# Kernel tuning notes

Hardware: AMD Instinct MI355X
Metric: run time of the kernel (lower is better)

The kernel has to match this reference:

```python
import jax, jax.numpy as jnp
import numpy as np

N_NODES = 100000
NFEAT = 256
NHID = 8
HEADS = 8
NCLASS = 32
N_EDGES = 1600000
NEG_SLOPE = 0.2


def setup_inputs() -> dict:
    key = jax.random.key(0)
    ks = jax.random.split(key, 10)
    glorot = lambda k, shape: jax.random.uniform(
        k, shape, jnp.float32, -1.0, 1.0) * np.sqrt(6.0 / (shape[0] + shape[-1]))
    x = jax.random.normal(ks[0], (N_NODES, NFEAT), jnp.float32)
    edge_index = jax.random.randint(ks[1], (2, N_EDGES), 0, N_NODES, jnp.int64)
    W1 = glorot(ks[2], (NFEAT, HEADS * NHID))
    a_src1 = glorot(ks[3], (HEADS, NHID))
    a_dst1 = glorot(ks[4], (HEADS, NHID))
    b1 = jnp.zeros((HEADS * NHID,), jnp.float32)
    W2 = glorot(ks[5], (HEADS * NHID, NCLASS))
    a_src2 = glorot(ks[6], (1, NCLASS))
    a_dst2 = glorot(ks[7], (1, NCLASS))
    b2 = jnp.zeros((NCLASS,), jnp.float32)
    return {"x": x, "edge_index": edge_index, "W1": W1, "a_src1": a_src1,
            "a_dst1": a_dst1, "b1": b1, "W2": W2, "a_src2": a_src2,
            "a_dst2": a_dst2, "b2": b2}


def gat_conv(x, src, dst, W, a_src, a_dst, b, heads, ch, concat):
    """One PyG-style GATConv layer (eval mode, self-loops already in src/dst)."""
    n = x.shape[0]
    h = (x @ W).reshape(n, heads, ch)                      # [N,H,C]
    al_s = jnp.einsum('nhc,hc->nh', h, a_src)              # [N,H]
    al_d = jnp.einsum('nhc,hc->nh', h, a_dst)              # [N,H]
    e = al_s[src] + al_d[dst]                              # [E,H]
    e = jnp.where(e >= 0, e, NEG_SLOPE * e)                # LeakyReLU(0.2)
    # segment softmax over destination node (self-loops => no empty segments)
    m = jax.ops.segment_max(e, dst, num_segments=n)
    e = jnp.exp(e - m[dst])
    s = jax.ops.segment_sum(e, dst, num_segments=n)
    alpha = e / (s[dst] + 1e-16)                           # [E,H]
    msg = h[src] * alpha[:, :, None]                       # [E,H,C]
    out = jax.ops.segment_sum(msg, dst, num_segments=n)    # [N,H,C]
    out = out.reshape(n, heads * ch) if concat else out.mean(axis=1)
    return out + b


def reference(x, edge_index, W1, a_src1, a_dst1, b1, W2, a_src2, a_dst2, b2):
    n = x.shape[0]
    loop = jnp.arange(n, dtype=edge_index.dtype)
    src = jnp.concatenate([edge_index[0], loop])
    dst = jnp.concatenate([edge_index[1], loop])
    h = gat_conv(x, src, dst, W1, a_src1, a_dst1, b1, HEADS, NHID, True)
    h = jax.nn.elu(h)
    out = gat_conv(h, src, dst, W2, a_src2, a_dst2, b2, 1, NCLASS, False)
    return jax.nn.log_softmax(out, axis=1)
```

## Files before the change

kernel.cpp:

```cpp
#include <hip/hip_runtime.h>
#include <math.h>

#define N_NODES 100000
#define NFEAT 256
#define D1 64
#define HEADS 8
#define NHID 8
#define NCLASS 32
#define NUM_EDGES 1600000
#define E_TOT 1700000
#define NEG_SLOPE 0.2f

#define BSHIFT 8
#define NBUCK 391
#define BCAP 5120
#define BIN_EPB 4096
#define BIN_EPT 16


#define OFF_H1    0
#define OFF_H2    6400000
#define OFF_ALS1  12800000
#define OFF_ALD1  13600000
#define OFF_ALS2  14400000
#define OFF_ALD2  14500000
#define OFF_BCUR  14600000
#define OFF_ROWP  14601024
#define OFF_CNT   14701024
#define OFF_BIN   14801024
#define OFF_CSR   16802944

typedef __attribute__((ext_vector_type(8))) short bf16x8;
typedef __attribute__((ext_vector_type(4))) float f32x4;

__device__ __forceinline__ float lrelu(float x) { return x >= 0.f ? x : NEG_SLOPE * x; }
__device__ __forceinline__ float fast_elu(float x) { return x > 0.f ? x : __expf(x) - 1.f; }

__device__ __forceinline__ unsigned f32_to_bf16_rne(float f) {
    unsigned u = __float_as_uint(f);
    return (u + 0x7fffu + ((u >> 16) & 1u)) >> 16;
}
__device__ __forceinline__ unsigned pack_bf16x2(float lo, float hi) {
    return f32_to_bf16_rne(lo) | (f32_to_bf16_rne(hi) << 16);
}
__device__ __forceinline__ float2 unpack_bf16x2(unsigned v) {
    return make_float2(__uint_as_float(v << 16), __uint_as_float(v & 0xffff0000u));
}

__device__ __forceinline__ void edge_src_dst(const int* __restrict__ ei, int e, int& src, int& dst) {
    if (e < NUM_EDGES) { src = ei[e]; dst = ei[NUM_EDGES + e]; }
    else { src = e - NUM_EDGES; dst = e - NUM_EDGES; }
}

__global__ __launch_bounds__(256) void gemm1_kernel(const float* __restrict__ x,
                                                    const float* __restrict__ W1,
                                                    const float* __restrict__ a_src,
                                                    const float* __restrict__ a_dst,
                                                    ushort* __restrict__ h1u,
                                                    float* __restrict__ als,
                                                    float* __restrict__ ald) {
    __shared__ unsigned xbf[2][64 * 20];
    const int tid = threadIdx.x;
    const int wv = tid >> 6;
    const int l = tid & 63;
    const int lm = l & 15;
    const int quad = l >> 4;
    const int r0 = blockIdx.x * 64;

    bf16x8 bfrag[8];
#pragma unroll
    for (int kb = 0; kb < 8; kb++)
#pragma unroll
        for (int j = 0; j < 8; j++) {
            const int k = kb * 32 + quad * 8 + j;
            bfrag[kb][j] = (short)f32_to_bf16_rne(W1[k * D1 + wv * 16 + lm]);
        }

    f32x4 acc[4];
#pragma unroll
    for (int s = 0; s < 4; s++) acc[s] = (f32x4)(0.f);

    const int sr = tid >> 2;
    const int sk = (tid & 3) * 8;
    const bool rok = (r0 + sr) < N_NODES;
    const float* xrow = &x[(size_t)(r0 + sr) * NFEAT];
    const int swrd = sr * 20 + (tid & 3) * 4;

    {
        uint4 pv = make_uint4(0, 0, 0, 0);
        if (rok) {
            const float4 va = *(const float4*)&xrow[sk];
            const float4 vb = *(const float4*)&xrow[sk + 4];
            pv.x = pack_bf16x2(va.x, va.y);
            pv.y = pack_bf16x2(va.z, va.w);
            pv.z = pack_bf16x2(vb.x, vb.y);
            pv.w = pack_bf16x2(vb.z, vb.w);
        }
        *(uint4*)&xbf[0][swrd] = pv;
    }
    __syncthreads();

#pragma unroll
    for (int kb = 0; kb < 8; kb++) {
        const int cur = kb & 1;
        const int nxt = cur ^ 1;
        float4 na = make_float4(0.f, 0.f, 0.f, 0.f);
        float4 nb = make_float4(0.f, 0.f, 0.f, 0.f);
        if (kb < 7 && rok) {
            na = *(const float4*)&xrow[(kb + 1) * 32 + sk];
            nb = *(const float4*)&xrow[(kb + 1) * 32 + sk + 4];
        }
#pragma unroll
        for (int s = 0; s < 4; s++) {
            const uint4 u = *(const uint4*)&xbf[cur][(s * 16 + lm) * 20 + quad * 4];
            const bf16x8 af = *(const bf16x8*)&u;
            acc[s] = __builtin_amdgcn_mfma_f32_16x16x32_bf16(af, bfrag[kb], acc[s], 0, 0, 0);
        }
        if (kb < 7) {
            uint4 pv;
            pv.x = pack_bf16x2(na.x, na.y);
            pv.y = pack_bf16x2(na.z, na.w);
            pv.z = pack_bf16x2(nb.x, nb.y);
            pv.w = pack_bf16x2(nb.z, nb.w);
            *(uint4*)&xbf[nxt][swrd] = pv;
            __syncthreads();
        }
    }

    const int head = wv * 2 + (lm >> 3);
    const int jc = l & 7;
    const float asl = a_src[head * NHID + jc];
    const float adl = a_dst[head * NHID + jc];
    const int col = wv * 16 + lm;
#pragma unroll
    for (int s = 0; s < 4; s++) {
#pragma unroll
        for (int r = 0; r < 4; r++) {
            const int row = r0 + s * 16 + quad * 4 + r;
            const float v = acc[s][r];
            float ps = v * asl, pd = v * adl;
            ps += __shfl_xor(ps, 1, 64); pd += __shfl_xor(pd, 1, 64);
            ps += __shfl_xor(ps, 2, 64); pd += __shfl_xor(pd, 2, 64);
            ps += __shfl_xor(ps, 4, 64); pd += __shfl_xor(pd, 4, 64);
            if (row < N_NODES) {
                h1u[(size_t)row * D1 + col] = (ushort)f32_to_bf16_rne(v);
                if (jc == 0) { als[row * HEADS + head] = ps; ald[row * HEADS + head] = pd; }
            }
        }
    }
}

__global__ __launch_bounds__(256) void bin_kernel(const int* __restrict__ ei,
                                                  int* __restrict__ bcur,
                                                  int* __restrict__ bin) {
    __shared__ int lcnt[NBUCK];
    __shared__ int lbase[NBUCK];
    const int tid = threadIdx.x;
    for (int b = tid; b < NBUCK; b += 256) lcnt[b] = 0;
    __syncthreads();
    const int e0 = blockIdx.x * BIN_EPB;
    int pk[BIN_EPT], bk[BIN_EPT], loff[BIN_EPT];
#pragma unroll
    for (int i = 0; i < BIN_EPT; i++) {
        const int e = e0 + i * 256 + tid;
        if (e < E_TOT) {
            int src, dst; edge_src_dst(ei, e, src, dst);
            bk[i] = dst >> BSHIFT;
            pk[i] = ((dst & 255) << 20) | src;
            loff[i] = atomicAdd(&lcnt[bk[i]], 1);
        } else bk[i] = -1;
    }
    __syncthreads();
    for (int b = tid; b < NBUCK; b += 256) {
        const int c = lcnt[b];
        lbase[b] = c ? atomicAdd(&bcur[b], c) : 0;
    }
    __syncthreads();
#pragma unroll
    for (int i = 0; i < BIN_EPT; i++) {
        if (bk[i] >= 0)
            bin[(size_t)bk[i] * BCAP + lbase[bk[i]] + loff[i]] = pk[i];
    }
}

__global__ __launch_bounds__(256) void bsort_kernel(const int* __restrict__ bcur,
                                                    const int* __restrict__ bin,
                                                    int* __restrict__ csr,
                                                    int* __restrict__ row_ptr,
                                                    int* __restrict__ cnt) {
    __shared__ int hcnt[256];
    __shared__ int hpre[256];
    __shared__ int cur[256];
    __shared__ int ssrc[BCAP];
    const int tid = threadIdx.x;
    const int bkt = blockIdx.x;
    const int cntb = bcur[bkt];
    const int base = bkt * BCAP;
    hcnt[tid] = 0;
    __syncthreads();
    for (int i = tid; i < cntb; i += 256)
        atomicAdd(&hcnt[bin[base + i] >> 20], 1);
    __syncthreads();
    const int myc = hcnt[tid];
    hpre[tid] = myc;
    __syncthreads();
    for (int off = 1; off < 256; off <<= 1) {
        const int t = (tid >= off) ? hpre[tid - off] : 0;
        __syncthreads();
        hpre[tid] += t;
        __syncthreads();
    }
    const int exc = hpre[tid] - myc;
    cur[tid] = exc;
    __syncthreads();
    for (int i = tid; i < cntb; i += 256) {
        const int v = bin[base + i];
        const int pos = atomicAdd(&cur[v >> 20], 1);
        ssrc[pos] = v & 0xFFFFF;
    }
    __syncthreads();
    for (int i = tid; i < cntb; i += 256) csr[base + i] = ssrc[i];
    const int n = (bkt << BSHIFT) + tid;
    if (n < N_NODES) { row_ptr[n] = base + exc; cnt[n] = myc; }
}

__global__ __launch_bounds__(256) void gather1_kernel(const int* __restrict__ row_ptr,
                                                      const int* __restrict__ cnt,
                                                      const int* __restrict__ csr_src,
                                                      const unsigned* __restrict__ h1b,
                                                      const float* __restrict__ als,
                                                      const float* __restrict__ ald,
                                                      const float* __restrict__ b1,
                                                      const float* __restrict__ W2,
                                                      const float* __restrict__ a_src2,
                                                      const float* __restrict__ a_dst2,
                                                      unsigned* __restrict__ h2b,
                                                      float* __restrict__ als2,
                                                      float* __restrict__ ald2) {
    __shared__ float zbuf[4][64];
    const int tid = threadIdx.x;
    const int wv = tid >> 6;
    const int n = blockIdx.x * 4 + wv;
    const int l = tid & 63;
    const int q = l >> 3;
    const int h = l & 7;
    const int start = row_ptr[n];
    const int deg = cnt[n];
    const float aldn = ald[n * HEADS + h];
    float a0 = 0.f, a1 = 0.f, a2 = 0.f, a3 = 0.f;
    float a4 = 0.f, a5 = 0.f, a6 = 0.f, a7 = 0.f, wsum = 0.f;

    int i = q;
    float e0 = 0.f, e1 = 0.f;
    uint4 u0 = make_uint4(0u, 0u, 0u, 0u);
    uint4 u1 = make_uint4(0u, 0u, 0u, 0u);
    int s2 = 0;
    if (i < deg) {
        const int s0 = csr_src[start + i];
        e0 = als[s0 * HEADS + h];
        u0 = *(const uint4*)&h1b[(size_t)s0 * 32 + h * 4];
    }
    if (i + 8 < deg) {
        const int s1 = csr_src[start + i + 8];
        e1 = als[s1 * HEADS + h];
        u1 = *(const uint4*)&h1b[(size_t)s1 * 32 + h * 4];
    }
    if (i + 16 < deg) s2 = csr_src[start + i + 16];

    for (; i < deg; i += 8) {
        int s3 = 0;
        if (i + 24 < deg) s3 = csr_src[start + i + 24];
        float e2 = 0.f;
        uint4 u2 = make_uint4(0u, 0u, 0u, 0u);
        if (i + 16 < deg) {
            e2 = als[s2 * HEADS + h];
            u2 = *(const uint4*)&h1b[(size_t)s2 * 32 + h * 4];
        }
        const float w = __expf(lrelu(e0 + aldn));
        const float2 p0 = unpack_bf16x2(u0.x);
        const float2 p1 = unpack_bf16x2(u0.y);
        const float2 p2 = unpack_bf16x2(u0.z);
        const float2 p3 = unpack_bf16x2(u0.w);
        a0 = fmaf(p0.x, w, a0); a1 = fmaf(p0.y, w, a1);
        a2 = fmaf(p1.x, w, a2); a3 = fmaf(p1.y, w, a3);
        a4 = fmaf(p2.x, w, a4); a5 = fmaf(p2.y, w, a5);
        a6 = fmaf(p3.x, w, a6); a7 = fmaf(p3.y, w, a7);
        wsum += w;
        e0 = e1; u0 = u1; e1 = e2; u1 = u2; s2 = s3;
    }

    a0 += __shfl_down(a0, 32, 64); a1 += __shfl_down(a1, 32, 64);
    a2 += __shfl_down(a2, 32, 64); a3 += __shfl_down(a3, 32, 64);
    a4 += __shfl_down(a4, 32, 64); a5 += __shfl_down(a5, 32, 64);
    a6 += __shfl_down(a6, 32, 64); a7 += __shfl_down(a7, 32, 64);
    wsum += __shfl_down(wsum, 32, 64);
    a0 += __shfl_down(a0, 16, 64); a1 += __shfl_down(a1, 16, 64);
    a2 += __shfl_down(a2, 16, 64); a3 += __shfl_down(a3, 16, 64);
    a4 += __shfl_down(a4, 16, 64); a5 += __shfl_down(a5, 16, 64);
    a6 += __shfl_down(a6, 16, 64); a7 += __shfl_down(a7, 16, 64);
    wsum += __shfl_down(wsum, 16, 64);
    a0 += __shfl_down(a0, 8, 64); a1 += __shfl_down(a1, 8, 64);
    a2 += __shfl_down(a2, 8, 64); a3 += __shfl_down(a3, 8, 64);
    a4 += __shfl_down(a4, 8, 64); a5 += __shfl_down(a5, 8, 64);
    a6 += __shfl_down(a6, 8, 64); a7 += __shfl_down(a7, 8, 64);
    wsum += __shfl_down(wsum, 8, 64);

    if (l < 8) {
        const float inv = 1.f / (wsum + 1e-16f);
        const float4 b1a = *(const float4*)&b1[l * 8];
        const float4 b1b = *(const float4*)&b1[l * 8 + 4];
        const float z0 = fast_elu(a0 * inv + b1a.x);
        const float z1 = fast_elu(a1 * inv + b1a.y);
        const float z2 = fast_elu(a2 * inv + b1a.z);
        const float z3 = fast_elu(a3 * inv + b1a.w);
        const float z4 = fast_elu(a4 * inv + b1b.x);
        const float z5 = fast_elu(a5 * inv + b1b.y);
        const float z6 = fast_elu(a6 * inv + b1b.z);
        const float z7 = fast_elu(a7 * inv + b1b.w);
        *(float4*)&zbuf[wv][l * 8]     = make_float4(z0, z1, z2, z3);
        *(float4*)&zbuf[wv][l * 8 + 4] = make_float4(z4, z5, z6, z7);
    }
    __builtin_amdgcn_wave_barrier();
    asm volatile("" ::: "memory");

    const int c = l & 31;
    const int kh = l >> 5;
    float y0 = 0.f, y1 = 0.f, y2 = 0.f, y3 = 0.f;
    const float* wbase = &W2[(kh * 32) * NCLASS + c];
#pragma unroll
    for (int j4 = 0; j4 < 2; j4++) {
        const int k0 = j4 * 16;
        const float4 za = *(const float4*)&zbuf[wv][kh * 32 + k0];
        const float4 zb = *(const float4*)&zbuf[wv][kh * 32 + k0 + 4];
        const float4 zc = *(const float4*)&zbuf[wv][kh * 32 + k0 + 8];
        const float4 zd = *(const float4*)&zbuf[wv][kh * 32 + k0 + 12];
        y0 = fmaf(za.x, wbase[(k0 + 0) * NCLASS], y0);
        y1 = fmaf(za.y, wbase[(k0 + 1) * NCLASS], y1);
        y2 = fmaf(za.z, wbase[(k0 + 2) * NCLASS], y2);
        y3 = fmaf(za.w, wbase[(k0 + 3) * NCLASS], y3);
        y0 = fmaf(zb.x, wbase[(k0 + 4) * NCLASS], y0);
        y1 = fmaf(zb.y, wbase[(k0 + 5) * NCLASS], y1);
        y2 = fmaf(zb.z, wbase[(k0 + 6) * NCLASS], y2);
        y3 = fmaf(zb.w, wbase[(k0 + 7) * NCLASS], y3);
        y0 = fmaf(zc.x, wbase[(k0 + 8) * NCLASS], y0);
        y1 = fmaf(zc.y, wbase[(k0 + 9) * NCLASS], y1);
        y2 = fmaf(zc.z, wbase[(k0 + 10) * NCLASS], y2);
        y3 = fmaf(zc.w, wbase[(k0 + 11) * NCLASS], y3);
        y0 = fmaf(zd.x, wbase[(k0 + 12) * NCLASS], y0);
        y1 = fmaf(zd.y, wbase[(k0 + 13) * NCLASS], y1);
        y2 = fmaf(zd.z, wbase[(k0 + 14) * NCLASS], y2);
        y3 = fmaf(zd.w, wbase[(k0 + 15) * NCLASS], y3);
    }
    float y = (y0 + y1) + (y2 + y3);
    y += __shfl_xor(y, 32, 64);

    float part = y * ((l < 32) ? a_src2[c] : a_dst2[c]);
    part += __shfl_xor(part, 1, 64);
    part += __shfl_xor(part, 2, 64);
    part += __shfl_xor(part, 4, 64);
    part += __shfl_xor(part, 8, 64);
    part += __shfl_xor(part, 16, 64);
    const float tdv = __shfl(part, 32, 64);
    if (l == 0) { als2[n] = part; ald2[n] = tdv; }

    const unsigned pw = pack_bf16x2(y, __shfl_down(y, 1, 64));
    if (l < 32 && (l & 1) == 0) h2b[(size_t)n * 16 + (l >> 1)] = pw;
}

__global__ __launch_bounds__(256) void gather2_kernel(const int* __restrict__ row_ptr,
                                                      const int* __restrict__ cnt,
                                                      const int* __restrict__ csr_src,
                                                      const unsigned* __restrict__ h2b,
                                                      const float* __restrict__ als2,
                                                      const float* __restrict__ ald2,
                                                      const float* __restrict__ b2,
                                                      float* __restrict__ out) {
    const int tid = threadIdx.x;
    const int n = blockIdx.x * 4 + (tid >> 6);
    const int l = tid & 63;
    const int q = l >> 2;
    const int c = l & 3;
    const int start = row_ptr[n];
    const int deg = cnt[n];
    const float aldn = ald2[n];
    float a0 = 0.f, a1 = 0.f, a2 = 0.f, a3 = 0.f;
    float a4 = 0.f, a5 = 0.f, a6 = 0.f, a7 = 0.f, wsum = 0.f;

    int i = q;
    float e0 = 0.f, e1 = 0.f;
    uint4 u0 = make_uint4(0u, 0u, 0u, 0u);
    uint4 u1 = make_uint4(0u, 0u, 0u, 0u);
    int s2 = 0;
    if (i < deg) {
        const int s0 = csr_src[start + i];
        e0 = als2[s0];
        u0 = *(const uint4*)&h2b[(size_t)s0 * 16 + c * 4];
    }
    if (i + 16 < deg) {
        const int s1 = csr_src[start + i + 16];
        e1 = als2[s1];
        u1 = *(const uint4*)&h2b[(size_t)s1 * 16 + c * 4];
    }
    if (i + 32 < deg) s2 = csr_src[start + i + 32];

    for (; i < deg; i += 16) {
        int s3 = 0;
        if (i + 48 < deg) s3 = csr_src[start + i + 48];
        float e2 = 0.f;
        uint4 u2 = make_uint4(0u, 0u, 0u, 0u);
        if (i + 32 < deg) {
            e2 = als2[s2];
            u2 = *(const uint4*)&h2b[(size_t)s2 * 16 + c * 4];
        }
        const float w = __expf(lrelu(e0 + aldn));
        const float2 p0 = unpack_bf16x2(u0.x);
        const float2 p1 = unpack_bf16x2(u0.y);
        const float2 p2 = unpack_bf16x2(u0.z);
        const float2 p3 = unpack_bf16x2(u0.w);
        a0 = fmaf(p0.x, w, a0); a1 = fmaf(p0.y, w, a1);
        a2 = fmaf(p1.x, w, a2); a3 = fmaf(p1.y, w, a3);
        a4 = fmaf(p2.x, w, a4); a5 = fmaf(p2.y, w, a5);
        a6 = fmaf(p3.x, w, a6); a7 = fmaf(p3.y, w, a7);
        wsum += w;
        e0 = e1; u0 = u1; e1 = e2; u1 = u2; s2 = s3;
    }

    a0 += __shfl_down(a0, 32, 64); a1 += __shfl_down(a1, 32, 64);
    a2 += __shfl_down(a2, 32, 64); a3 += __shfl_down(a3, 32, 64);
    a4 += __shfl_down(a4, 32, 64); a5 += __shfl_down(a5, 32, 64);
    a6 += __shfl_down(a6, 32, 64); a7 += __shfl_down(a7, 32, 64);
    wsum += __shfl_down(wsum, 32, 64);
    a0 += __shfl_down(a0, 16, 64); a1 += __shfl_down(a1, 16, 64);
    a2 += __shfl_down(a2, 16, 64); a3 += __shfl_down(a3, 16, 64);
    a4 += __shfl_down(a4, 16, 64); a5 += __shfl_down(a5, 16, 64);
    a6 += __shfl_down(a6, 16, 64); a7 += __shfl_down(a7, 16, 64);
    wsum += __shfl_down(wsum, 16, 64);
    a0 += __shfl_down(a0, 8, 64); a1 += __shfl_down(a1, 8, 64);
    a2 += __shfl_down(a2, 8, 64); a3 += __shfl_down(a3, 8, 64);
    a4 += __shfl_down(a4, 8, 64); a5 += __shfl_down(a5, 8, 64);
    a6 += __shfl_down(a6, 8, 64); a7 += __shfl_down(a7, 8, 64);
    wsum += __shfl_down(wsum, 8, 64);
    a0 += __shfl_down(a0, 4, 64); a1 += __shfl_down(a1, 4, 64);
    a2 += __shfl_down(a2, 4, 64); a3 += __shfl_down(a3, 4, 64);
    a4 += __shfl_down(a4, 4, 64); a5 += __shfl_down(a5, 4, 64);
    a6 += __shfl_down(a6, 4, 64); a7 += __shfl_down(a7, 4, 64);
    wsum += __shfl_down(wsum, 4, 64);

    const float inv = 1.f / (wsum + 1e-16f);
    const float4 b2a = *(const float4*)&b2[c * 8];
    const float4 b2b = *(const float4*)&b2[c * 8 + 4];
    const float v0 = a0 * inv + b2a.x, v1 = a1 * inv + b2a.y;
    const float v2 = a2 * inv + b2a.z, v3 = a3 * inv + b2a.w;
    const float v4 = a4 * inv + b2b.x, v5 = a5 * inv + b2b.y;
    const float v6 = a6 * inv + b2b.z, v7 = a7 * inv + b2b.w;
    float mx = fmaxf(fmaxf(fmaxf(v0, v1), fmaxf(v2, v3)),
                     fmaxf(fmaxf(v4, v5), fmaxf(v6, v7)));
    mx = fmaxf(mx, __shfl_xor(mx, 1, 64));
    mx = fmaxf(mx, __shfl_xor(mx, 2, 64));
    float s = __expf(v0 - mx) + __expf(v1 - mx) + __expf(v2 - mx) + __expf(v3 - mx)
            + __expf(v4 - mx) + __expf(v5 - mx) + __expf(v6 - mx) + __expf(v7 - mx);
    s += __shfl_xor(s, 1, 64);
    s += __shfl_xor(s, 2, 64);
    const float lse = mx + logf(s);
    if (l < 4) {
        float* op = &out[(size_t)n * NCLASS + c * 8];
        *(float4*)&op[0] = make_float4(v0 - lse, v1 - lse, v2 - lse, v3 - lse);
        *(float4*)&op[4] = make_float4(v4 - lse, v5 - lse, v6 - lse, v7 - lse);
    }
}

extern "C" void kernel_launch(void* const* d_in, const int* in_sizes, int n_in,
                              void* d_out, int out_size, void* d_ws, size_t ws_size,
                              hipStream_t stream) {
    const float* x      = (const float*)d_in[0];
    const int*   ei     = (const int*)d_in[1];
    const float* W1     = (const float*)d_in[2];
    const float* a_src1 = (const float*)d_in[3];
    const float* a_dst1 = (const float*)d_in[4];
    const float* b1     = (const float*)d_in[5];
    const float* W2     = (const float*)d_in[6];
    const float* a_src2 = (const float*)d_in[7];
    const float* a_dst2 = (const float*)d_in[8];
    const float* b2     = (const float*)d_in[9];
    float* out = (float*)d_out;
    float* ws  = (float*)d_ws;

    ushort* h1u     = (ushort*)(ws + OFF_H1);
    unsigned* h1b   = (unsigned*)(ws + OFF_H1);
    unsigned* h2b   = (unsigned*)(ws + OFF_H2);
    float* als1     = ws + OFF_ALS1;
    float* ald1     = ws + OFF_ALD1;
    float* als2     = ws + OFF_ALS2;
    float* ald2     = ws + OFF_ALD2;
    int*   bcur     = (int*)(ws + OFF_BCUR);
    int*   row_ptr  = (int*)(ws + OFF_ROWP);
    int*   cnt      = (int*)(ws + OFF_CNT);
    int*   bin      = (int*)(ws + OFF_BIN);
    int*   csr      = (int*)(ws + OFF_CSR);

    hipMemsetAsync(bcur, 0, NBUCK * sizeof(int), stream);

    gemm1_kernel<<<(N_NODES + 63) / 64, 256, 0, stream>>>(x, W1, a_src1, a_dst1, h1u, als1, ald1);
    bin_kernel<<<(E_TOT + BIN_EPB - 1) / BIN_EPB, 256, 0, stream>>>(ei, bcur, bin);
    bsort_kernel<<<NBUCK, 256, 0, stream>>>(bcur, bin, csr, row_ptr, cnt);
    gather1_kernel<<<N_NODES / 4, 256, 0, stream>>>(row_ptr, cnt, csr, h1b, als1, ald1,
                                                    b1, W2, a_src2, a_dst2, h2b, als2, ald2);
    gather2_kernel<<<N_NODES / 4, 256, 0, stream>>>(row_ptr, cnt, csr, h2b, als2, ald2, b2, out);
}
```

Measured before the change: 337.0 us.

## Merge GEMM1 and bucket sort into one launch, unroll gather loops

Moves bin_kernel ahead of the GEMM and combines gemm1 and bsort into a single kernel. The first NBUCK blocks do the per-bucket sort and the rest do the 64-row GEMM tiles, sharing one shared-memory buffer. The aim is to run the small, latency-bound sort alongside the GEMM and drop one launch. It also adds unroll 2 to the gather loops. Risks: the shared-memory footprint is now the maximum of both paths (about 23 KB for every block, where the GEMM alone used about 10 KB), which can lower GEMM occupancy, and the unroll raises register pressure.

```diff
diff --git a/kernel.cpp b/kernel.cpp
--- a/kernel.cpp
+++ b/kernel.cpp
@@ -16,6 +16,7 @@
 #define BCAP 5120
 #define BIN_EPB 4096
 #define BIN_EPT 16
+#define GEMM1_NB 1563
 
 
 #define OFF_H1    0
@@ -52,20 +53,97 @@
     else { src = e - NUM_EDGES; dst = e - NUM_EDGES; }
 }
 
-__global__ __launch_bounds__(256) void gemm1_kernel(const float* __restrict__ x,
-                                                    const float* __restrict__ W1,
-                                                    const float* __restrict__ a_src,
-                                                    const float* __restrict__ a_dst,
-                                                    ushort* __restrict__ h1u,
-                                                    float* __restrict__ als,
-                                                    float* __restrict__ ald) {
-    __shared__ unsigned xbf[2][64 * 20];
+__global__ __launch_bounds__(256) void bin_kernel(const int* __restrict__ ei,
+                                                  int* __restrict__ bcur,
+                                                  int* __restrict__ bin) {
+    __shared__ int lcnt[NBUCK];
+    __shared__ int lbase[NBUCK];
     const int tid = threadIdx.x;
+    for (int b = tid; b < NBUCK; b += 256) lcnt[b] = 0;
+    __syncthreads();
+    const int e0 = blockIdx.x * BIN_EPB;
+    int pk[BIN_EPT], bk[BIN_EPT], loff[BIN_EPT];
+#pragma unroll
+    for (int i = 0; i < BIN_EPT; i++) {
+        const int e = e0 + i * 256 + tid;
+        if (e < E_TOT) {
+            int src, dst; edge_src_dst(ei, e, src, dst);
+            bk[i] = dst >> BSHIFT;
+            pk[i] = ((dst & 255) << 20) | src;
+            loff[i] = atomicAdd(&lcnt[bk[i]], 1);
+        } else bk[i] = -1;
+    }
+    __syncthreads();
+    for (int b = tid; b < NBUCK; b += 256) {
+        const int c = lcnt[b];
+        lbase[b] = c ? atomicAdd(&bcur[b], c) : 0;
+    }
+    __syncthreads();
+#pragma unroll
+    for (int i = 0; i < BIN_EPT; i++) {
+        if (bk[i] >= 0)
+            bin[(size_t)bk[i] * BCAP + lbase[bk[i]] + loff[i]] = pk[i];
+    }
+}
+
+__global__ __launch_bounds__(256) void gemm1_bsort_kernel(const float* __restrict__ x,
+                                                          const float* __restrict__ W1,
+                                                          const float* __restrict__ a_src,
+                                                          const float* __restrict__ a_dst,
+                                                          ushort* __restrict__ h1u,
+                                                          float* __restrict__ als,
+                                                          float* __restrict__ ald,
+                                                          const int* __restrict__ bcur,
+                                                          const int* __restrict__ bin,
+                                                          int* __restrict__ csr,
+                                                          int* __restrict__ row_ptr,
+                                                          int* __restrict__ cnt) {
+    __shared__ __align__(16) unsigned char smem[23552];
+    const int tid = threadIdx.x;
+
+    if (blockIdx.x < NBUCK) {
+        int* hcnt = (int*)smem;
+        int* hpre = hcnt + 256;
+        int* curp = hpre + 256;
+        int* ssrc = curp + 256;
+        const int bkt = blockIdx.x;
+        const int cntb = bcur[bkt];
+        const int base = bkt * BCAP;
+        hcnt[tid] = 0;
+        __syncthreads();
+        for (int i = tid; i < cntb; i += 256)
+            atomicAdd(&hcnt[bin[base + i] >> 20], 1);
+        __syncthreads();
+        const int myc = hcnt[tid];
+        hpre[tid] = myc;
+        __syncthreads();
+        for (int off = 1; off < 256; off <<= 1) {
+            const int t = (tid >= off) ? hpre[tid - off] : 0;
+            __syncthreads();
+            hpre[tid] += t;
+            __syncthreads();
+        }
+        const int exc = hpre[tid] - myc;
+        curp[tid] = exc;
+        __syncthreads();
+        for (int i = tid; i < cntb; i += 256) {
+            const int v = bin[base + i];
+            const int pos = atomicAdd(&curp[v >> 20], 1);
+            ssrc[pos] = v & 0xFFFFF;
+        }
+        __syncthreads();
+        for (int i = tid; i < cntb; i += 256) csr[base + i] = ssrc[i];
+        const int n = (bkt << BSHIFT) + tid;
+        if (n < N_NODES) { row_ptr[n] = base + exc; cnt[n] = myc; }
+        return;
+    }
+
+    unsigned* xbf = (unsigned*)smem;
     const int wv = tid >> 6;
     const int l = tid & 63;
     const int lm = l & 15;
     const int quad = l >> 4;
-    const int r0 = blockIdx.x * 64;
+    const int r0 = (blockIdx.x - NBUCK) * 64;
 
     bf16x8 bfrag[8];
 #pragma unroll
@@ -96,7 +174,7 @@
             pv.z = pack_bf16x2(vb.x, vb.y);
             pv.w = pack_bf16x2(vb.z, vb.w);
         }
-        *(uint4*)&xbf[0][swrd] = pv;
+        *(uint4*)&xbf[swrd] = pv;
     }
     __syncthreads();
 
@@ -112,7 +190,7 @@
         }
 #pragma unroll
         for (int s = 0; s < 4; s++) {
-            const uint4 u = *(const uint4*)&xbf[cur][(s * 16 + lm) * 20 + quad * 4];
+            const uint4 u = *(const uint4*)&xbf[cur * 1280 + (s * 16 + lm) * 20 + quad * 4];
             const bf16x8 af = *(const bf16x8*)&u;
             acc[s] = __builtin_amdgcn_mfma_f32_16x16x32_bf16(af, bfrag[kb], acc[s], 0, 0, 0);
         }
@@ -122,7 +200,7 @@
             pv.y = pack_bf16x2(na.z, na.w);
             pv.z = pack_bf16x2(nb.x, nb.y);
             pv.w = pack_bf16x2(nb.z, nb.w);
-            *(uint4*)&xbf[nxt][swrd] = pv;
+            *(uint4*)&xbf[nxt * 1280 + swrd] = pv;
             __syncthreads();
         }
     }
@@ -148,80 +226,6 @@
             }
         }
     }
-}
-
-__global__ __launch_bounds__(256) void bin_kernel(const int* __restrict__ ei,
-                                                  int* __restrict__ bcur,
-                                                  int* __restrict__ bin) {
-    __shared__ int lcnt[NBUCK];
-    __shared__ int lbase[NBUCK];
-    const int tid = threadIdx.x;
-    for (int b = tid; b < NBUCK; b += 256) lcnt[b] = 0;
-    __syncthreads();
-    const int e0 = blockIdx.x * BIN_EPB;
-    int pk[BIN_EPT], bk[BIN_EPT], loff[BIN_EPT];
-#pragma unroll
-    for (int i = 0; i < BIN_EPT; i++) {
-        const int e = e0 + i * 256 + tid;
-        if (e < E_TOT) {
-            int src, dst; edge_src_dst(ei, e, src, dst);
-            bk[i] = dst >> BSHIFT;
-            pk[i] = ((dst & 255) << 20) | src;
-            loff[i] = atomicAdd(&lcnt[bk[i]], 1);
-        } else bk[i] = -1;
-    }
-    __syncthreads();
-    for (int b = tid; b < NBUCK; b += 256) {
-        const int c = lcnt[b];
-        lbase[b] = c ? atomicAdd(&bcur[b], c) : 0;
-    }
-    __syncthreads();
-#pragma unroll
-    for (int i = 0; i < BIN_EPT; i++) {
-        if (bk[i] >= 0)
-            bin[(size_t)bk[i] * BCAP + lbase[bk[i]] + loff[i]] = pk[i];
-    }
-}
-
-__global__ __launch_bounds__(256) void bsort_kernel(const int* __restrict__ bcur,
-                                                    const int* __restrict__ bin,
-                                                    int* __restrict__ csr,
-                                                    int* __restrict__ row_ptr,
-                                                    int* __restrict__ cnt) {
-    __shared__ int hcnt[256];
-    __shared__ int hpre[256];
-    __shared__ int cur[256];
-    __shared__ int ssrc[BCAP];
-    const int tid = threadIdx.x;
-    const int bkt = blockIdx.x;
-    const int cntb = bcur[bkt];
-    const int base = bkt * BCAP;
-    hcnt[tid] = 0;
-    __syncthreads();
-    for (int i = tid; i < cntb; i += 256)
-        atomicAdd(&hcnt[bin[base + i] >> 20], 1);
-    __syncthreads();
-    const int myc = hcnt[tid];
-    hpre[tid] = myc;
-    __syncthreads();
-    for (int off = 1; off < 256; off <<= 1) {
-        const int t = (tid >= off) ? hpre[tid - off] : 0;
-        __syncthreads();
-        hpre[tid] += t;
-        __syncthreads();
-    }
-    const int exc = hpre[tid] - myc;
-    cur[tid] = exc;
-    __syncthreads();
-    for (int i = tid; i < cntb; i += 256) {
-        const int v = bin[base + i];
-        const int pos = atomicAdd(&cur[v >> 20], 1);
-        ssrc[pos] = v & 0xFFFFF;
-    }
-    __syncthreads();
-    for (int i = tid; i < cntb; i += 256) csr[base + i] = ssrc[i];
-    const int n = (bkt << BSHIFT) + tid;
-    if (n < N_NODES) { row_ptr[n] = base + exc; cnt[n] = myc; }
 }
 
 __global__ __launch_bounds__(256) void gather1_kernel(const int* __restrict__ row_ptr,
@@ -267,6 +271,7 @@
     }
     if (i + 16 < deg) s2 = csr_src[start + i + 16];
 
+#pragma unroll 2
     for (; i < deg; i += 8) {
         int s3 = 0;
         if (i + 24 < deg) s3 = csr_src[start + i + 24];
@@ -403,6 +408,7 @@
     }
     if (i + 32 < deg) s2 = csr_src[start + i + 32];
 
+#pragma unroll 2
     for (; i < deg; i += 16) {
         int s3 = 0;
         if (i + 48 < deg) s3 = csr_src[start + i + 48];
@@ -500,9 +506,10 @@
 
     hipMemsetAsync(bcur, 0, NBUCK * sizeof(int), stream);
 
-    gemm1_kernel<<<(N_NODES + 63) / 64, 256, 0, stream>>>(x, W1, a_src1, a_dst1, h1u, als1, ald1);
     bin_kernel<<<(E_TOT + BIN_EPB - 1) / BIN_EPB, 256, 0, stream>>>(ei, bcur, bin);
-    bsort_kernel<<<NBUCK, 256, 0, stream>>>(bcur, bin, csr, row_ptr, cnt);
+    gemm1_bsort_kernel<<<NBUCK + GEMM1_NB, 256, 0, stream>>>(x, W1, a_src1, a_dst1,
+                                                             h1u, als1, ald1,
+                                                             bcur, bin, csr, row_ptr, cnt);
     gather1_kernel<<<N_NODES / 4, 256, 0, stream>>>(row_ptr, cnt, csr, h1b, als1, ald1,
                                                     b1, W2, a_src2, a_dst2, h2b, als2, ald2);
     gather2_kernel<<<N_NODES / 4, 256, 0, stream>>>(row_ptr, cnt, csr, h2b, als2, ald2, b2, out);
```

Result: faster. 329.4 us (-2.3%).
